# Optimization experiments

Hardware: AMD Instinct MI355X
Metric: run time of the kernel (lower is better)

## Reference

```python
import jax, jax.numpy as jnp
import numpy as np

VOCAB = 400000
DIM = 128        # meta['embed_dim']
NBITS = 2        # bits per code
CODEBOOK = 1 << NBITS   # 4 codebook entries
MASK = CODEBOOK - 1
N_WORDS = VOCAB * DIM * NBITS // 32  # 3,200,000 packed int32 words


def setup_inputs() -> dict:
    key = jax.random.key(0)
    k1, k2, k3 = jax.random.split(key, 3)
    input_ids = jax.random.randint(k1, (64, 4096), 0, VOCAB, dtype=jnp.int64)
    # packed bit array: nonnegative int32 words (top bit clear so >> is logical)
    bit_arr = jax.random.randint(k2, (N_WORDS,), 0, 2147483647, dtype=jnp.int32)
    codebook = jax.random.normal(k3, (CODEBOOK,), dtype=jnp.float32)
    return {"input": input_ids, "bit_arr": bit_arr, "codebook": codebook}


def reference(input, bit_arr, codebook):
    flat = input.reshape(-1).astype(jnp.int32)            # [N]
    # code position for (token, dim): p = token*DIM + dim
    pos = flat[:, None] * DIM + jnp.arange(DIM, dtype=jnp.int32)[None, :]  # [N, DIM]
    bitpos = pos * NBITS
    word = bitpos >> 5            # // 32
    shift = bitpos & 31           # % 32
    codes = (bit_arr[word] >> shift) & MASK               # [N, DIM] in [0, 2^NBITS)
    embeds = codebook[codes]                              # [N, DIM] fp32
    return embeds.reshape(input.shape + (DIM,))
```

## Files before the change

kernel.cpp:

```cpp
#include <hip/hip_runtime.h>
#include <hip/hip_bf16.h>


#define EMB_DIM 128

typedef float vfloat4 __attribute__((ext_vector_type(4)));

__global__ __launch_bounds__(256, 8) void embed2bit_kernel(
    const int* __restrict__ ids,
    const int* __restrict__ bits,
    const float* __restrict__ cb,
    float* __restrict__ out,
    int n_tokens)
{
    const long long n_items = (long long)n_tokens * 32;
    const long long stride  = (long long)gridDim.x * blockDim.x;
    long long gid = (long long)blockIdx.x * blockDim.x + threadIdx.x;

    float c0 = cb[0], c1 = cb[1], c2 = cb[2], c3 = cb[3];

    for (long long base = gid; base < n_items; base += 4 * stride) {
        long long idx[4];
        int tok[4], wrd[4];
        bool ok[4];

#pragma unroll
        for (int j = 0; j < 4; ++j) {
            idx[j] = base + (long long)j * stride;
            ok[j]  = idx[j] < n_items;
            tok[j] = ok[j] ? ids[idx[j] >> 5] : 0;
        }
#pragma unroll
        for (int j = 0; j < 4; ++j) {
            int k  = (int)(idx[j] & 31);
            wrd[j] = ok[j] ? bits[(long long)tok[j] * 8 + (k >> 2)] : 0;
        }
#pragma unroll
        for (int j = 0; j < 4; ++j) {
            if (!ok[j]) continue;
            int k    = (int)(idx[j] & 31);
            int byte = (wrd[j] >> ((k & 3) * 8)) & 0xff;
            vfloat4 r;
#pragma unroll
            for (int q = 0; q < 4; ++q) {
                int c    = (byte >> (2 * q)) & 3;
                float lo = (c & 1) ? c1 : c0;
                float hi = (c & 1) ? c3 : c2;
                r[q]     = (c & 2) ? hi : lo;
            }
            long long t = idx[j] >> 5;
            __builtin_nontemporal_store(
                r, reinterpret_cast<vfloat4*>(out + t * EMB_DIM + k * 4));
        }
    }
}

extern "C" void kernel_launch(void* const* d_in, const int* in_sizes, int n_in,
                              void* d_out, int out_size, void* d_ws, size_t ws_size,
                              hipStream_t stream) {
    const int*   ids  = (const int*)d_in[0];
    const int*   bits = (const int*)d_in[1];
    const float* cb   = (const float*)d_in[2];
    float*       out  = (float*)d_out;

    int n_tokens = in_sizes[0];
    long long n_items = (long long)n_tokens * 32;

    int block = 256;
    long long want = (n_items + block - 1) / block;
    int grid = (int)(want < 2048 ? want : 2048);

    embed2bit_kernel<<<grid, block, 0, stream>>>(ids, bits, cb, out, n_tokens);
}
```

Baseline: 163.8 us.

## Software-pipeline id and codeword loads across grid-stride iterations

```diff
diff --git a/kernel.cpp b/kernel.cpp
--- a/kernel.cpp
+++ b/kernel.cpp
@@ -3,43 +3,65 @@
 
 
 #define EMB_DIM 128
+#define BLOCK 256
+#define GRID  1024
+#define BATCH 4
 
 typedef float vfloat4 __attribute__((ext_vector_type(4)));
 
-__global__ __launch_bounds__(256, 8) void embed2bit_kernel(
+__global__ __launch_bounds__(BLOCK) void embed2bit_pipe_kernel(
     const int* __restrict__ ids,
     const int* __restrict__ bits,
     const float* __restrict__ cb,
     float* __restrict__ out,
-    int n_tokens)
+    int n_items)
 {
-    const long long n_items = (long long)n_tokens * 32;
-    const long long stride  = (long long)gridDim.x * blockDim.x;
-    long long gid = (long long)blockIdx.x * blockDim.x + threadIdx.x;
+    const long long stride = (long long)gridDim.x * blockDim.x;
+    const long long tid0   = (long long)blockIdx.x * blockDim.x + threadIdx.x;
+    const long long step   = (long long)BATCH * stride;
 
-    float c0 = cb[0], c1 = cb[1], c2 = cb[2], c3 = cb[3];
+    if (tid0 >= n_items) return;
 
-    for (long long base = gid; base < n_items; base += 4 * stride) {
-        long long idx[4];
-        int tok[4], wrd[4];
-        bool ok[4];
+    const float c0 = cb[0], c1 = cb[1], c2 = cb[2], c3 = cb[3];
+    const long long last = n_items - 1;
+
+    int tokC[BATCH], tokN[BATCH], wC[BATCH];
 
 #pragma unroll
-        for (int j = 0; j < 4; ++j) {
-            idx[j] = base + (long long)j * stride;
-            ok[j]  = idx[j] < n_items;
-            tok[j] = ok[j] ? ids[idx[j] >> 5] : 0;
+    for (int j = 0; j < BATCH; ++j) {
+        long long i = tid0 + (long long)j * stride; if (i > last) i = last;
+        tokC[j] = ids[i >> 5];
+    }
+#pragma unroll
+    for (int j = 0; j < BATCH; ++j) {
+        long long i = tid0 + step + (long long)j * stride; if (i > last) i = last;
+        tokN[j] = ids[i >> 5];
+    }
+#pragma unroll
+    for (int j = 0; j < BATCH; ++j) {
+        long long i = tid0 + (long long)j * stride; if (i > last) i = last;
+        wC[j] = bits[(long long)tokC[j] * 8 + ((i & 31) >> 2)];
+    }
+
+    for (long long base = tid0; base < n_items; base += step) {
+        int tokF[BATCH], wN[BATCH];
+#pragma unroll
+        for (int j = 0; j < BATCH; ++j) {
+            long long i = base + 2 * step + (long long)j * stride;
+            if (i > last) i = last;
+            tokF[j] = ids[i >> 5];
         }
 #pragma unroll
-        for (int j = 0; j < 4; ++j) {
-            int k  = (int)(idx[j] & 31);
-            wrd[j] = ok[j] ? bits[(long long)tok[j] * 8 + (k >> 2)] : 0;
+        for (int j = 0; j < BATCH; ++j) {
+            long long i = base + step + (long long)j * stride;
+            if (i > last) i = last;
+            wN[j] = bits[(long long)tokN[j] * 8 + ((i & 31) >> 2)];
         }
 #pragma unroll
-        for (int j = 0; j < 4; ++j) {
-            if (!ok[j]) continue;
-            int k    = (int)(idx[j] & 31);
-            int byte = (wrd[j] >> ((k & 3) * 8)) & 0xff;
+        for (int j = 0; j < BATCH; ++j) {
+            long long i = base + (long long)j * stride;
+            if (i >= n_items) break;
+            int byte = (wC[j] >> (((int)i & 3) * 8)) & 0xff;
             vfloat4 r;
 #pragma unroll
             for (int q = 0; q < 4; ++q) {
@@ -48,10 +70,10 @@
                 float hi = (c & 1) ? c3 : c2;
                 r[q]     = (c & 2) ? hi : lo;
             }
-            long long t = idx[j] >> 5;
-            __builtin_nontemporal_store(
-                r, reinterpret_cast<vfloat4*>(out + t * EMB_DIM + k * 4));
+            *reinterpret_cast<vfloat4*>(out + i * 4) = r;
         }
+#pragma unroll
+        for (int j = 0; j < BATCH; ++j) { wC[j] = wN[j]; tokN[j] = tokF[j]; }
     }
 }
 
@@ -64,11 +86,10 @@
     float*       out  = (float*)d_out;
 
     int n_tokens = in_sizes[0];
-    long long n_items = (long long)n_tokens * 32;
+    int n_items  = n_tokens * 32;
 
-    int block = 256;
-    long long want = (n_items + block - 1) / block;
-    int grid = (int)(want < 2048 ? want : 2048);
+    long long want = ((long long)n_items + BLOCK - 1) / BLOCK;
+    int grid = (int)(want < GRID ? want : GRID);
 
-    embed2bit_kernel<<<grid, block, 0, stream>>>(ids, bits, cb, out, n_tokens);
+    embed2bit_pipe_kernel<<<grid, BLOCK, 0, stream>>>(ids, bits, cb, out, n_items);
 }
```

New measurement: 156.3 us. 1.05x faster.
